# Performance work log

Hardware: AMD Instinct MI355X
Metric: run time of the kernel (lower is better)

Reference implementation:

```python
import jax, jax.numpy as jnp
import numpy as np

B, S, DIM = 8, 1, 2048
H = 16
QLR, KVLR = 1536, 512
DN, DR, DV = 128, 64, 128      # qk_nope, qk_rope, v head dims
START = 8191                    # start_pos; end_pos = START + S = 8192
EPS = 1e-6
SCALE = (DN + DR) ** -0.5


def _rms(x, w):
    # F.rms_norm: x / sqrt(mean(x^2)+eps) * w
    return x * w * jax.lax.rsqrt(jnp.mean(jnp.square(x), axis=-1, keepdims=True) + EPS)


def _rope(x, cos, sin):
    # x: [..., r]; consecutive pairs (x0,x1) treated as complex, multiplied by cos+i*sin
    xr, xi = x[..., 0::2], x[..., 1::2]
    out_r = xr * cos - xi * sin
    out_i = xr * sin + xi * cos
    return jnp.stack([out_r, out_i], axis=-1).reshape(x.shape)


def setup_inputs() -> dict:
    key = jax.random.key(0)
    ks = jax.random.split(key, 12)
    # rotary tables for the single decode position
    inv_freq = 1.0 / (10000.0 ** (np.arange(0, DR, 2, dtype=np.float32) / DR))  # [DR/2]
    pos = np.arange(START, START + S, dtype=np.float32)[:, None]                # [S,1]
    ang = pos * inv_freq[None, :]                                               # [S, DR/2]
    return {
        "x": jax.random.normal(ks[0], (B, S, DIM), jnp.float32),
        "start_pos": START,
        "freqs_cos": jnp.asarray(np.cos(ang)),
        "freqs_sin": jnp.asarray(np.sin(ang)),
        "kv_cache_prefix": jax.random.normal(ks[1], (B, START, KVLR), jnp.float32),
        "pe_cache_prefix": jax.random.normal(ks[2], (B, START, DR), jnp.float32),
        "wq_a_w": jax.random.normal(ks[3], (QLR, DIM), jnp.float32) * 0.02,
        "wq_a_b": jnp.zeros((QLR,), jnp.float32),
        "q_norm_w": jnp.ones((QLR,), jnp.float32),
        "wq_b_w": jax.random.normal(ks[4], (H * (DN + DR), QLR), jnp.float32) * 0.02,
        "wq_b_b": jnp.zeros((H * (DN + DR),), jnp.float32),
        "wkv_a_w": jax.random.normal(ks[5], (KVLR + DR, DIM), jnp.float32) * 0.02,
        "wkv_a_b": jnp.zeros((KVLR + DR,), jnp.float32),
        "kv_norm_w": jnp.ones((KVLR,), jnp.float32),
        "wkv_b_w": jax.random.normal(ks[6], (H * (DN + DV), KVLR), jnp.float32) * 0.02,
        "wo_w": jax.random.normal(ks[7], (DIM, H * DV), jnp.float32) * 0.02,
        "wo_b": jnp.zeros((DIM,), jnp.float32),
    }


def reference(x, start_pos, freqs_cos, freqs_sin, kv_cache_prefix, pe_cache_prefix,
              wq_a_w, wq_a_b, q_norm_w, wq_b_w, wq_b_b,
              wkv_a_w, wkv_a_b, kv_norm_w, wkv_b_w, wo_w, wo_b):
    b, s, _ = x.shape
    # low-rank query projection
    q = _rms(x @ wq_a_w.T + wq_a_b, q_norm_w) @ wq_b_w.T + wq_b_b
    q = q.reshape(b, s, H, DN + DR)
    q_nope, q_pe = q[..., :DN], q[..., DN:]
    cos = freqs_cos[None, :, None, :]  # [1,s,1,DR/2]
    sin = freqs_sin[None, :, None, :]
    q_pe = _rope(q_pe, cos, sin)
    # compressed KV + rope key branch
    kvpe = x @ wkv_a_w.T + wkv_a_b               # [b,s,KVLR+DR]
    kv, k_pe = kvpe[..., :KVLR], kvpe[..., KVLR:]
    k_pe = _rope(k_pe[:, :, None, :], cos, sin)[:, :, 0, :]
    # weight absorption: project q_nope into latent space through wkv_b's K-part
    wkv_b = wkv_b_w.reshape(H, DN + DV, KVLR)
    q_abs = jnp.einsum('bshd,hdc->bshc', q_nope, wkv_b[:, :DN])
    # append current step to caches
    kv_cache = jnp.concatenate([kv_cache_prefix, _rms(kv, kv_norm_w)], axis=1)  # [b,t,KVLR]
    pe_cache = jnp.concatenate([pe_cache_prefix, k_pe], axis=1)                 # [b,t,DR]
    # attention in latent space (seqlen=1 decode -> no causal mask needed)
    scores = (jnp.einsum('bshc,btc->bsht', q_abs, kv_cache)
              + jnp.einsum('bshr,btr->bsht', q_pe, pe_cache)) * SCALE
    attn = jax.nn.softmax(scores.astype(jnp.float32), axis=-1).astype(x.dtype)
    out = jnp.einsum('bsht,btc->bshc', attn, kv_cache)
    out = jnp.einsum('bshc,hdc->bshd', out, wkv_b[:, DN:])  # V-part of wkv_b
    return out.reshape(b, s, H * DV) @ wo_w.T + wo_b
```

## Files before the change

kernel.cpp:

```cpp
#include <hip/hip_runtime.h>
#include <math.h>

namespace {
constexpr int B_   = 8;
constexpr int DIM_ = 2048;
constexpr int H_   = 16;
constexpr int QLR_ = 1536;
constexpr int KVLR_= 512;
constexpr int DN_  = 128;
constexpr int DR_  = 64;
constexpr int DV_  = 128;
constexpr int TPRE_= 8191;
constexpr int CE_  = 576;
constexpr int NCH_ = 32;
constexpr int CT_  = 256;
constexpr int TS_  = 32;
constexpr int PSTR_= 20;
constexpr float EPS_ = 1e-6f;
constexpr float SCALE_ = 0.07216878364870322f;

constexpr size_t WS_QLAT  = 0;
constexpr size_t WS_KVPE  = WS_QLAT  + (size_t)B_*QLR_;
constexpr size_t WS_KVNEW = WS_KVPE  + (size_t)B_*CE_;
constexpr size_t WS_PENEW = WS_KVNEW + (size_t)B_*KVLR_;
constexpr size_t WS_SSQ   = WS_PENEW + (size_t)B_*DR_;
constexpr size_t WS_QNOPE = WS_SSQ   + 16;
constexpr size_t WS_QT    = WS_QNOPE + (size_t)B_*H_*DN_;
constexpr size_t WS_MLOC  = WS_QT    + (size_t)B_*CE_*H_;
constexpr size_t WS_LLOC  = WS_MLOC  + (size_t)B_*H_*NCH_;
constexpr size_t WS_OUT2  = WS_LLOC  + (size_t)B_*H_*NCH_;
constexpr size_t WS_OPART = WS_OUT2  + (size_t)B_*DIM_;
}

__device__ __forceinline__ void gload16(const float* src, float* ldsDst) {
  __builtin_amdgcn_global_load_lds((const __attribute__((address_space(1))) void*)src,
                                   (__attribute__((address_space(3))) void*)ldsDst,
                                   16, 0, 0);
}

__device__ __forceinline__ float rsum16(float v) {
  int x = __float_as_int(v);
  v += __int_as_float(__builtin_amdgcn_update_dpp(0, x, 0xB1, 0xF, 0xF, true));
  x = __float_as_int(v);
  v += __int_as_float(__builtin_amdgcn_update_dpp(0, x, 0x4E, 0xF, 0xF, true));
  x = __float_as_int(v);
  v += __int_as_float(__builtin_amdgcn_update_dpp(0, x, 0x141, 0xF, 0xF, true));
  x = __float_as_int(v);
  v += __int_as_float(__builtin_amdgcn_update_dpp(0, x, 0x140, 0xF, 0xF, true));
  return v;
}

__global__ __launch_bounds__(256) void mla_k1(const float* __restrict__ x,
                                              const float* __restrict__ wqa,
                                              const float* __restrict__ bqa,
                                              const float* __restrict__ wkva,
                                              const float* __restrict__ bkva,
                                              const float* __restrict__ fcos,
                                              const float* __restrict__ fsin,
                                              float* __restrict__ ws) {
  __shared__ float red[4 * B_];
  const int w = threadIdx.x >> 6, l = threadIdx.x & 63;
  const int r0 = (blockIdx.x * 4 + w) * 2;
  const float* W; const float* bias; int rr;
  if (r0 < QLR_) { W = wqa;  bias = bqa;  rr = r0; }
  else           { W = wkva; bias = bkva; rr = r0 - QLR_; }
  const float4* w0p = (const float4*)(W + (size_t)rr * DIM_);
  const float4* w1p = (const float4*)(W + (size_t)(rr + 1) * DIM_);
  const float4* x4  = (const float4*)x;
  float4 wv0[8], wv1[8];
#pragma unroll
  for (int j = 0; j < 8; ++j) { wv0[j] = w0p[l + 64 * j]; wv1[j] = w1p[l + 64 * j]; }
  float acc0[B_], acc1[B_];
#pragma unroll
  for (int b = 0; b < B_; ++b) { acc0[b] = 0.f; acc1[b] = 0.f; }
#pragma unroll
  for (int b = 0; b < B_; ++b) {
#pragma unroll
    for (int j = 0; j < 8; ++j) {
      const float4 xv = x4[b * (DIM_ / 4) + l + 64 * j];
      acc0[b] = fmaf(wv0[j].x, xv.x, fmaf(wv0[j].y, xv.y, fmaf(wv0[j].z, xv.z, fmaf(wv0[j].w, xv.w, acc0[b]))));
      acc1[b] = fmaf(wv1[j].x, xv.x, fmaf(wv1[j].y, xv.y, fmaf(wv1[j].z, xv.z, fmaf(wv1[j].w, xv.w, acc1[b]))));
    }
  }
#pragma unroll
  for (int b = 0; b < B_; ++b)
#pragma unroll
    for (int s = 32; s; s >>= 1) {
      acc0[b] += __shfl_xor(acc0[b], s);
      acc1[b] += __shfl_xor(acc1[b], s);
    }
  const int rblk = blockIdx.x * 8;
  if (l == 0) {
    const float b0 = bias[rr], b1 = bias[rr + 1];
    if (r0 < QLR_) {
      float* out = ws + WS_QLAT;
#pragma unroll
      for (int b = 0; b < B_; ++b) {
        const float v0 = acc0[b] + b0, v1 = acc1[b] + b1;
        out[b * QLR_ + r0]     = v0;
        out[b * QLR_ + r0 + 1] = v1;
        red[w * B_ + b] = v0 * v0 + v1 * v1;
      }
    } else if (rr < KVLR_) {
      float* out = ws + WS_KVPE;
#pragma unroll
      for (int b = 0; b < B_; ++b) {
        const float v0 = acc0[b] + b0, v1 = acc1[b] + b1;
        out[b * CE_ + rr]     = v0;
        out[b * CE_ + rr + 1] = v1;
        red[w * B_ + b] = v0 * v0 + v1 * v1;
      }
    } else {
      const int i = (rr - KVLR_) >> 1;
      const float c = fcos[i], s = fsin[i];
      float* pen = ws + WS_PENEW;
#pragma unroll
      for (int b = 0; b < B_; ++b) {
        const float xr = acc0[b] + b0, xi = acc1[b] + b1;
        pen[b * DR_ + 2 * i]     = xr * c - xi * s;
        pen[b * DR_ + 2 * i + 1] = xr * s + xi * c;
      }
    }
  }
  if (rblk < QLR_ + KVLR_) {
    __syncthreads();
    if (threadIdx.x < B_) {
      const float sacc = red[0 * B_ + threadIdx.x] + red[1 * B_ + threadIdx.x] +
                         red[2 * B_ + threadIdx.x] + red[3 * B_ + threadIdx.x];
      atomicAdd(&ws[WS_SSQ + (rblk >= QLR_ ? B_ : 0) + threadIdx.x], sacc);
    }
  }
}

__global__ __launch_bounds__(256) void mla_k3(const float* __restrict__ qnw,
                                              const float* __restrict__ wqb,
                                              const float* __restrict__ bqb,
                                              const float* __restrict__ fcos,
                                              const float* __restrict__ fsin,
                                              float* __restrict__ ws) {
  const int w = threadIdx.x >> 6, l = threadIdx.x & 63;
  const int r0 = blockIdx.x * 8 + w * 2;
  const float4* w0p = (const float4*)(wqb + (size_t)r0 * QLR_);
  const float4* w1p = (const float4*)(wqb + (size_t)(r0 + 1) * QLR_);
  const float4* g4  = (const float4*)qnw;
  const float4* x4  = (const float4*)(ws + WS_QLAT);
  float4 wg0[6], wg1[6];
#pragma unroll
  for (int j = 0; j < 6; ++j) {
    const int c4 = l + 64 * j;
    const float4 a = w0p[c4], bb = w1p[c4], g = g4[c4];
    wg0[j].x = a.x * g.x; wg0[j].y = a.y * g.y; wg0[j].z = a.z * g.z; wg0[j].w = a.w * g.w;
    wg1[j].x = bb.x * g.x; wg1[j].y = bb.y * g.y; wg1[j].z = bb.z * g.z; wg1[j].w = bb.w * g.w;
  }
  float acc0[B_], acc1[B_];
#pragma unroll
  for (int b = 0; b < B_; ++b) { acc0[b] = 0.f; acc1[b] = 0.f; }
#pragma unroll
  for (int b = 0; b < B_; ++b) {
#pragma unroll
    for (int j = 0; j < 6; ++j) {
      const float4 xv = x4[b * (QLR_ / 4) + l + 64 * j];
      acc0[b] = fmaf(wg0[j].x, xv.x, fmaf(wg0[j].y, xv.y, fmaf(wg0[j].z, xv.z, fmaf(wg0[j].w, xv.w, acc0[b]))));
      acc1[b] = fmaf(wg1[j].x, xv.x, fmaf(wg1[j].y, xv.y, fmaf(wg1[j].z, xv.z, fmaf(wg1[j].w, xv.w, acc1[b]))));
    }
  }
#pragma unroll
  for (int b = 0; b < B_; ++b)
#pragma unroll
    for (int s = 32; s; s >>= 1) {
      acc0[b] += __shfl_xor(acc0[b], s);
      acc1[b] += __shfl_xor(acc1[b], s);
    }
  if (l == 0) {
    const int h = r0 / (DN_ + DR_);
    const int j0 = r0 - h * (DN_ + DR_);
    const float b0 = bqb[r0], b1 = bqb[r0 + 1];
    if (j0 < DN_) {
      float* qn = ws + WS_QNOPE;
#pragma unroll
      for (int b = 0; b < B_; ++b) {
        const float sb = 1.0f / sqrtf(ws[WS_SSQ + b] / (float)QLR_ + EPS_);
        qn[(b * H_ + h) * DN_ + j0]     = acc0[b] * sb + b0;
        qn[(b * H_ + h) * DN_ + j0 + 1] = acc1[b] * sb + b1;
      }
    } else {
      const int i = (j0 - DN_) >> 1;
      const float c = fcos[i], s = fsin[i];
      float* qTT = ws + WS_QT;
#pragma unroll
      for (int b = 0; b < B_; ++b) {
        const float sb = 1.0f / sqrtf(ws[WS_SSQ + b] / (float)QLR_ + EPS_);
        const float xr = acc0[b] * sb + b0, xi = acc1[b] * sb + b1;
        qTT[((size_t)(b * H_ + h)) * CE_ + KVLR_ + 2 * i]     = xr * c - xi * s;
        qTT[((size_t)(b * H_ + h)) * CE_ + KVLR_ + 2 * i + 1] = xr * s + xi * c;
      }
    }
  }
}

__global__ __launch_bounds__(256) void mla_k4(const float* __restrict__ wkvb,
                                              float* __restrict__ ws) {
  __shared__ float red[7 * 32 * B_];
  const int h = blockIdx.y;
  const int strip = blockIdx.x;
  const int tid = threadIdx.x;
  const int c = tid & 31, dg = tid >> 5;
  const int cg = strip * 32 + c;
  const float* qn = ws + WS_QNOPE;
  float acc[B_];
#pragma unroll
  for (int b = 0; b < B_; ++b) acc[b] = 0.f;
  const float* wp = wkvb + (size_t)h * 256 * KVLR_ + cg;
#pragma unroll
  for (int dd = 0; dd < 16; ++dd) {
    const int d = dg * 16 + dd;
    const float wv = wp[(size_t)d * KVLR_];
#pragma unroll
    for (int b = 0; b < B_; ++b) acc[b] = fmaf(qn[(b * H_ + h) * DN_ + d], wv, acc[b]);
  }
  if (dg > 0) {
#pragma unroll
    for (int b = 0; b < B_; ++b) red[(((dg - 1) * 32) + c) * B_ + b] = acc[b];
  }
  __syncthreads();
  if (dg == 0) {
    float* qTT = ws + WS_QT;
#pragma unroll
    for (int b = 0; b < B_; ++b) {
      float v = acc[b];
#pragma unroll
      for (int g = 0; g < 7; ++g) v += red[(g * 32 + c) * B_ + b];
      qTT[((size_t)(b * H_ + h)) * CE_ + cg] = v;
    }
  }
}

__global__ __launch_bounds__(512) void mla_k5(const float* __restrict__ kvpre,
                                              const float* __restrict__ pepre,
                                              const float* __restrict__ kvnw,
                                              float* __restrict__ ws) {
  __shared__ float kv_lds[2][TS_ * CE_];
  __shared__ float p_lds[TS_ * PSTR_];
  __shared__ float m_st[H_], l_st[H_], f_st[H_];

  const int b = blockIdx.y, chunk = blockIdx.x;
  const int t0 = chunk * CT_;
  const int tid = threadIdx.x;
  const int w = tid >> 6, l = tid & 63;
  const int cs = l & 15;
  const int hl = l >> 4;
  const int tg = w >> 1;
  const int hg = (w & 1) * 4 + hl;
  const int c4p = tid >> 2, h4p = tid & 3;

  const float* kvraw = ws + WS_KVPE + b * CE_;
  const float* penew = ws + WS_PENEW + b * DR_;

  auto stageKV = [&](float* buf, int s) {
    const int ts0 = t0 + s * TS_;
#pragma unroll
    for (int k = 0; k < 9; ++k) {
      const int i = w + 8 * k;
      const int f = i * 64 + l;
      const int tl = f / 144;
      const int c4 = f - tl * 144;
      const int tgl = ts0 + tl;
      const float* src;
      if (tgl < TPRE_) {
        src = (c4 < 128) ? (kvpre + ((size_t)b * TPRE_ + tgl) * KVLR_ + 4 * c4)
                         : (pepre + ((size_t)b * TPRE_ + tgl) * DR_ + 4 * (c4 - 128));
      } else {
        src = (c4 < 128) ? (kvraw + 4 * c4) : (penew + 4 * (c4 - 128));
      }
      gload16(src, buf + (size_t)i * 64 * 4);
    }
  };

  stageKV(kv_lds[0], 0);

  float4 q0v[9], q1v[9];
  {
    const float* qb0 = ws + WS_QT + ((size_t)(b * H_) + 2 * hg) * CE_ + cs * 36;
    const float* qb1 = qb0 + CE_;
#pragma unroll
    for (int j = 0; j < 9; ++j) {
      q0v[j] = *(const float4*)(qb0 + 4 * j);
      q1v[j] = *(const float4*)(qb1 + 4 * j);
    }
  }
  if (tid < H_) { m_st[tid] = -3.4e38f; l_st[tid] = 0.f; }

  float o[4][4];
#pragma unroll
  for (int cc = 0; cc < 4; ++cc)
#pragma unroll
    for (int hh = 0; hh < 4; ++hh) o[cc][hh] = 0.f;

  for (int s = 0; s < CT_ / TS_; ++s) {
    __syncthreads();
    if (s + 1 < CT_ / TS_) stageKV(kv_lds[(s + 1) & 1], s + 1);
    float* bufc = kv_lds[s & 1];

    if (chunk == NCH_ - 1 && s == CT_ / TS_ - 1) {
      const float sck = 1.0f / sqrtf(ws[WS_SSQ + B_ + b] / (float)KVLR_ + EPS_);
      float* row = bufc + (TS_ - 1) * CE_;
      row[tid] = row[tid] * kvnw[tid] * sck;
      __syncthreads();
    }

    {
      const float* kb = bufc + (tg * 8) * CE_ + cs * 36;
#pragma unroll
      for (int tt = 0; tt < 8; ++tt) {
        const float* kr = kb + tt * CE_;
        float a0 = 0.f, a1 = 0.f;
#pragma unroll
        for (int j = 0; j < 9; ++j) {
          const float4 k = *(const float4*)(kr + 4 * j);
          const float4 qa = q0v[j], qc = q1v[j];
          a0 = fmaf(k.x, qa.x, fmaf(k.y, qa.y, fmaf(k.z, qa.z, fmaf(k.w, qa.w, a0))));
          a1 = fmaf(k.x, qc.x, fmaf(k.y, qc.y, fmaf(k.z, qc.z, fmaf(k.w, qc.w, a1))));
        }
        a0 = rsum16(a0);
        a1 = rsum16(a1);
        if (cs == 0) {
          float2 v; v.x = a0 * SCALE_; v.y = a1 * SCALE_;
          *(float2*)(p_lds + (tg * 8 + tt) * PSTR_ + 2 * hg) = v;
        }
      }
    }
    __syncthreads();

    {
      const int h2 = tid >> 5, tl2 = tid & 31;
      const float sv = p_lds[tl2 * PSTR_ + h2];
      float msub = sv;
#pragma unroll
      for (int d = 16; d; d >>= 1) msub = fmaxf(msub, __shfl_xor(msub, d, 32));
      const float mold = m_st[h2];
      const float mnew = fmaxf(mold, msub);
      const float e = __expf(sv - mnew);
      float lsum = e;
#pragma unroll
      for (int d = 16; d; d >>= 1) lsum += __shfl_xor(lsum, d, 32);
      p_lds[tl2 * PSTR_ + h2] = e;
      if (tl2 == 0) {
        const float fac = __expf(mold - mnew);
        f_st[h2] = fac;
        l_st[h2] = l_st[h2] * fac + lsum;
        m_st[h2] = mnew;
      }
    }
    __syncthreads();

    {
      const float4 fv = *(const float4*)(f_st + 4 * h4p);
#pragma unroll
      for (int cc = 0; cc < 4; ++cc) {
        o[cc][0] *= fv.x; o[cc][1] *= fv.y; o[cc][2] *= fv.z; o[cc][3] *= fv.w;
      }
#pragma unroll 8
      for (int t = 0; t < TS_; ++t) {
        const float4 kq = *(const float4*)(bufc + t * CE_ + 4 * c4p);
        const float4 pq = *(const float4*)(p_lds + t * PSTR_ + 4 * h4p);
        o[0][0] = fmaf(pq.x, kq.x, o[0][0]); o[0][1] = fmaf(pq.y, kq.x, o[0][1]);
        o[0][2] = fmaf(pq.z, kq.x, o[0][2]); o[0][3] = fmaf(pq.w, kq.x, o[0][3]);
        o[1][0] = fmaf(pq.x, kq.y, o[1][0]); o[1][1] = fmaf(pq.y, kq.y, o[1][1]);
        o[1][2] = fmaf(pq.z, kq.y, o[1][2]); o[1][3] = fmaf(pq.w, kq.y, o[1][3]);
        o[2][0] = fmaf(pq.x, kq.z, o[2][0]); o[2][1] = fmaf(pq.y, kq.z, o[2][1]);
        o[2][2] = fmaf(pq.z, kq.z, o[2][2]); o[2][3] = fmaf(pq.w, kq.z, o[2][3]);
        o[3][0] = fmaf(pq.x, kq.w, o[3][0]); o[3][1] = fmaf(pq.y, kq.w, o[3][1]);
        o[3][2] = fmaf(pq.z, kq.w, o[3][2]); o[3][3] = fmaf(pq.w, kq.w, o[3][3]);
      }
    }
  }

  {
    float* Op = ws + WS_OPART;
#pragma unroll
    for (int hh = 0; hh < 4; ++hh) {
      const int h = 4 * h4p + hh;
      float4 v;
      v.x = o[0][hh]; v.y = o[1][hh]; v.z = o[2][hh]; v.w = o[3][hh];
      *(float4*)(Op + ((size_t)(b * H_ + h) * NCH_ + chunk) * KVLR_ + 4 * c4p) = v;
    }
    if (tid < H_) {
      ws[WS_MLOC + (b * H_ + tid) * NCH_ + chunk] = m_st[tid];
      ws[WS_LLOC + (b * H_ + tid) * NCH_ + chunk] = l_st[tid];
    }
  }
}

__global__ __launch_bounds__(256) void mla_k6(const float* __restrict__ wkvb,
                                              float* __restrict__ ws) {
  const int h = blockIdx.x, b = blockIdx.y;
  __shared__ float wgt[NCH_];
  __shared__ float ao[KVLR_];
  __shared__ float Linv;
  const int tid = threadIdx.x;
  if (tid < NCH_) {
    const float m = ws[WS_MLOC + (b * H_ + h) * NCH_ + tid];
    float M = m;
#pragma unroll
    for (int s = 16; s; s >>= 1) M = fmaxf(M, __shfl_xor(M, s, 32));
    const float wv = __expf(m - M);
    wgt[tid] = wv;
    float lv = ws[WS_LLOC + (b * H_ + h) * NCH_ + tid] * wv;
#pragma unroll
    for (int s = 16; s; s >>= 1) lv += __shfl_xor(lv, s, 32);
    if (tid == 0) Linv = 1.0f / lv;
  }
  __syncthreads();
  const float* Ob = ws + WS_OPART + (size_t)(b * H_ + h) * NCH_ * KVLR_;
  float s0 = 0.f, s1 = 0.f;
#pragma unroll 4
  for (int i = 0; i < NCH_; ++i) {
    const float wv = wgt[i];
    s0 = fmaf(wv, Ob[(size_t)i * KVLR_ + tid], s0);
    s1 = fmaf(wv, Ob[(size_t)i * KVLR_ + tid + 256], s1);
  }
  const float li = Linv;
  ao[tid] = s0 * li;
  ao[tid + 256] = s1 * li;
  __syncthreads();

  const int w6 = tid >> 6, l6 = tid & 63;
  const float4 ax = *(const float4*)(ao + 4 * l6);
  const float4 bx = *(const float4*)(ao + 256 + 4 * l6);
  float* out2 = ws + WS_OUT2 + b * DIM_ + h * DV_;
#pragma unroll 2
  for (int k = 0; k < 32; k += 2) {
    const int v0 = w6 * 32 + k;
    const float4* w20 = (const float4*)(wkvb + ((size_t)h * 256 + DN_ + v0) * KVLR_);
    const float4* w21 = (const float4*)(wkvb + ((size_t)h * 256 + DN_ + v0 + 1) * KVLR_);
    const float4 a0 = w20[l6], c0 = w20[64 + l6];
    const float4 a1 = w21[l6], c1 = w21[64 + l6];
    float t0 = fmaf(a0.x, ax.x, fmaf(a0.y, ax.y, fmaf(a0.z, ax.z, fmaf(a0.w, ax.w,
               fmaf(c0.x, bx.x, fmaf(c0.y, bx.y, fmaf(c0.z, bx.z, c0.w * bx.w)))))));
    float t1 = fmaf(a1.x, ax.x, fmaf(a1.y, ax.y, fmaf(a1.z, ax.z, fmaf(a1.w, ax.w,
               fmaf(c1.x, bx.x, fmaf(c1.y, bx.y, fmaf(c1.z, bx.z, c1.w * bx.w)))))));
#pragma unroll
    for (int d = 32; d; d >>= 1) {
      t0 += __shfl_xor(t0, d);
      t1 += __shfl_xor(t1, d);
    }
    if (l6 == 0) { out2[v0] = t0; out2[v0 + 1] = t1; }
  }
}

__global__ __launch_bounds__(256) void mla_k7(const float* __restrict__ wo,
                                              const float* __restrict__ wob,
                                              const float* __restrict__ ws,
                                              float* __restrict__ out) {
  const int w = threadIdx.x >> 6, l = threadIdx.x & 63;
  const int r0 = (blockIdx.x * 4 + w) * 2;
  const float4* w0p = (const float4*)(wo + (size_t)r0 * DIM_);
  const float4* w1p = (const float4*)(wo + (size_t)(r0 + 1) * DIM_);
  const float4* x4  = (const float4*)(ws + WS_OUT2);
  float4 wv0[8], wv1[8];
#pragma unroll
  for (int j = 0; j < 8; ++j) { wv0[j] = w0p[l + 64 * j]; wv1[j] = w1p[l + 64 * j]; }
  float acc0[B_], acc1[B_];
#pragma unroll
  for (int b = 0; b < B_; ++b) { acc0[b] = 0.f; acc1[b] = 0.f; }
#pragma unroll
  for (int b = 0; b < B_; ++b) {
#pragma unroll
    for (int j = 0; j < 8; ++j) {
      const float4 xv = x4[b * (DIM_ / 4) + l + 64 * j];
      acc0[b] = fmaf(wv0[j].x, xv.x, fmaf(wv0[j].y, xv.y, fmaf(wv0[j].z, xv.z, fmaf(wv0[j].w, xv.w, acc0[b]))));
      acc1[b] = fmaf(wv1[j].x, xv.x, fmaf(wv1[j].y, xv.y, fmaf(wv1[j].z, xv.z, fmaf(wv1[j].w, xv.w, acc1[b]))));
    }
  }
#pragma unroll
  for (int b = 0; b < B_; ++b)
#pragma unroll
    for (int s = 32; s; s >>= 1) {
      acc0[b] += __shfl_xor(acc0[b], s);
      acc1[b] += __shfl_xor(acc1[b], s);
    }
  if (l == 0) {
    const float b0 = wob[r0], b1 = wob[r0 + 1];
#pragma unroll
    for (int b = 0; b < B_; ++b) {
      out[b * DIM_ + r0]     = acc0[b] + b0;
      out[b * DIM_ + r0 + 1] = acc1[b] + b1;
    }
  }
}

extern "C" void kernel_launch(void* const* d_in, const int* in_sizes, int n_in,
                              void* d_out, int out_size, void* d_ws, size_t ws_size,
                              hipStream_t stream) {
  (void)in_sizes; (void)n_in; (void)out_size; (void)ws_size;
  const float* x     = (const float*)d_in[0];
  const float* fcos  = (const float*)d_in[2];
  const float* fsin  = (const float*)d_in[3];
  const float* kvpre = (const float*)d_in[4];
  const float* pepre = (const float*)d_in[5];
  const float* wqa   = (const float*)d_in[6];
  const float* bqa   = (const float*)d_in[7];
  const float* qnw   = (const float*)d_in[8];
  const float* wqb   = (const float*)d_in[9];
  const float* bqb   = (const float*)d_in[10];
  const float* wkva  = (const float*)d_in[11];
  const float* bkva  = (const float*)d_in[12];
  const float* kvnw  = (const float*)d_in[13];
  const float* wkvb  = (const float*)d_in[14];
  const float* wo    = (const float*)d_in[15];
  const float* wob   = (const float*)d_in[16];
  float* ws  = (float*)d_ws;
  float* out = (float*)d_out;

  hipMemsetAsync((char*)d_ws + WS_SSQ * sizeof(float), 0, 16 * sizeof(float), stream);
  mla_k1<<<dim3((QLR_ + CE_) / 8), dim3(256), 0, stream>>>(x, wqa, bqa, wkva, bkva, fcos, fsin, ws);
  mla_k3<<<dim3(H_ * (DN_ + DR_) / 8), dim3(256), 0, stream>>>(qnw, wqb, bqb, fcos, fsin, ws);
  mla_k4<<<dim3(16, H_), dim3(256), 0, stream>>>(wkvb, ws);
  mla_k5<<<dim3(NCH_, B_), dim3(512), 0, stream>>>(kvpre, pepre, kvnw, ws);
  mla_k6<<<dim3(H_, B_), dim3(256), 0, stream>>>(wkvb, ws);
  mla_k7<<<dim3(DIM_ / 8), dim3(256), 0, stream>>>(wo, wob, ws, out);
}
```

Before: 351.2 us.

## Double attention chunk count and recompute RMS norms locally instead of atomics

The attention split-K kernel now uses 64 chunks of 128 tokens with 16-token stages, doubling the number of blocks over the KV cache to raise parallelism and shrink LDS per stage. The RMS sum-of-squares atomics and the memset are removed; instead each consumer block recomputes the q and kv norm scales from the workspace. Some barriers are replaced with a lighter lgkm-wait barrier. The trade-offs are redundant norm reductions in every block and more partials to merge in the combine kernel.

```diff
diff --git a/kernel.cpp b/kernel.cpp
--- a/kernel.cpp
+++ b/kernel.cpp
@@ -12,19 +12,18 @@
 constexpr int DV_  = 128;
 constexpr int TPRE_= 8191;
 constexpr int CE_  = 576;
-constexpr int NCH_ = 32;
-constexpr int CT_  = 256;
-constexpr int TS_  = 32;
+constexpr int NCH_ = 64;
+constexpr int CT_  = 128;
+constexpr int TS_  = 16;
+constexpr int NS_  = CT_ / TS_;
 constexpr int PSTR_= 20;
 constexpr float EPS_ = 1e-6f;
 constexpr float SCALE_ = 0.07216878364870322f;
 
 constexpr size_t WS_QLAT  = 0;
 constexpr size_t WS_KVPE  = WS_QLAT  + (size_t)B_*QLR_;
-constexpr size_t WS_KVNEW = WS_KVPE  + (size_t)B_*CE_;
-constexpr size_t WS_PENEW = WS_KVNEW + (size_t)B_*KVLR_;
-constexpr size_t WS_SSQ   = WS_PENEW + (size_t)B_*DR_;
-constexpr size_t WS_QNOPE = WS_SSQ   + 16;
+constexpr size_t WS_PENEW = WS_KVPE  + (size_t)B_*CE_;
+constexpr size_t WS_QNOPE = WS_PENEW + (size_t)B_*DR_;
 constexpr size_t WS_QT    = WS_QNOPE + (size_t)B_*H_*DN_;
 constexpr size_t WS_MLOC  = WS_QT    + (size_t)B_*CE_*H_;
 constexpr size_t WS_LLOC  = WS_MLOC  + (size_t)B_*H_*NCH_;
@@ -50,6 +49,12 @@
   return v;
 }
 
+__device__ __forceinline__ void barrier_lgkm() {
+  asm volatile("s_waitcnt lgkmcnt(0)" ::: "memory");
+  __builtin_amdgcn_s_barrier();
+  __builtin_amdgcn_sched_barrier(0);
+}
+
 __global__ __launch_bounds__(256) void mla_k1(const float* __restrict__ x,
                                               const float* __restrict__ wqa,
                                               const float* __restrict__ bqa,
@@ -58,7 +63,6 @@
                                               const float* __restrict__ fcos,
                                               const float* __restrict__ fsin,
                                               float* __restrict__ ws) {
-  __shared__ float red[4 * B_];
   const int w = threadIdx.x >> 6, l = threadIdx.x & 63;
   const int r0 = (blockIdx.x * 4 + w) * 2;
   const float* W; const float* bias; int rr;
@@ -89,26 +93,21 @@
       acc0[b] += __shfl_xor(acc0[b], s);
       acc1[b] += __shfl_xor(acc1[b], s);
     }
-  const int rblk = blockIdx.x * 8;
   if (l == 0) {
     const float b0 = bias[rr], b1 = bias[rr + 1];
     if (r0 < QLR_) {
       float* out = ws + WS_QLAT;
 #pragma unroll
       for (int b = 0; b < B_; ++b) {
-        const float v0 = acc0[b] + b0, v1 = acc1[b] + b1;
-        out[b * QLR_ + r0]     = v0;
-        out[b * QLR_ + r0 + 1] = v1;
-        red[w * B_ + b] = v0 * v0 + v1 * v1;
+        out[b * QLR_ + r0]     = acc0[b] + b0;
+        out[b * QLR_ + r0 + 1] = acc1[b] + b1;
       }
     } else if (rr < KVLR_) {
       float* out = ws + WS_KVPE;
 #pragma unroll
       for (int b = 0; b < B_; ++b) {
-        const float v0 = acc0[b] + b0, v1 = acc1[b] + b1;
-        out[b * CE_ + rr]     = v0;
-        out[b * CE_ + rr + 1] = v1;
-        red[w * B_ + b] = v0 * v0 + v1 * v1;
+        out[b * CE_ + rr]     = acc0[b] + b0;
+        out[b * CE_ + rr + 1] = acc1[b] + b1;
       }
     } else {
       const int i = (rr - KVLR_) >> 1;
@@ -120,14 +119,6 @@
         pen[b * DR_ + 2 * i]     = xr * c - xi * s;
         pen[b * DR_ + 2 * i + 1] = xr * s + xi * c;
       }
-    }
-  }
-  if (rblk < QLR_ + KVLR_) {
-    __syncthreads();
-    if (threadIdx.x < B_) {
-      const float sacc = red[0 * B_ + threadIdx.x] + red[1 * B_ + threadIdx.x] +
-                         red[2 * B_ + threadIdx.x] + red[3 * B_ + threadIdx.x];
-      atomicAdd(&ws[WS_SSQ + (rblk >= QLR_ ? B_ : 0) + threadIdx.x], sacc);
     }
   }
 }
@@ -138,7 +129,23 @@
                                               const float* __restrict__ fcos,
                                               const float* __restrict__ fsin,
                                               float* __restrict__ ws) {
-  const int w = threadIdx.x >> 6, l = threadIdx.x & 63;
+  __shared__ float qs_s[B_];
+  const int tid = threadIdx.x;
+  {
+    const int bq = tid >> 5, l32 = tid & 31;
+    const float4* ql4 = (const float4*)(ws + WS_QLAT + (size_t)bq * QLR_);
+    float ss = 0.f;
+#pragma unroll
+    for (int j = 0; j < 12; ++j) {
+      const float4 v = ql4[l32 + 32 * j];
+      ss = fmaf(v.x, v.x, fmaf(v.y, v.y, fmaf(v.z, v.z, fmaf(v.w, v.w, ss))));
+    }
+#pragma unroll
+    for (int d = 16; d; d >>= 1) ss += __shfl_xor(ss, d, 32);
+    if (l32 == 0) qs_s[bq] = 1.0f / sqrtf(ss / (float)QLR_ + EPS_);
+    __syncthreads();
+  }
+  const int w = tid >> 6, l = tid & 63;
   const int r0 = blockIdx.x * 8 + w * 2;
   const float4* w0p = (const float4*)(wqb + (size_t)r0 * QLR_);
   const float4* w1p = (const float4*)(wqb + (size_t)(r0 + 1) * QLR_);
@@ -179,7 +186,7 @@
       float* qn = ws + WS_QNOPE;
 #pragma unroll
       for (int b = 0; b < B_; ++b) {
-        const float sb = 1.0f / sqrtf(ws[WS_SSQ + b] / (float)QLR_ + EPS_);
+        const float sb = qs_s[b];
         qn[(b * H_ + h) * DN_ + j0]     = acc0[b] * sb + b0;
         qn[(b * H_ + h) * DN_ + j0 + 1] = acc1[b] * sb + b1;
       }
@@ -189,7 +196,7 @@
       float* qTT = ws + WS_QT;
 #pragma unroll
       for (int b = 0; b < B_; ++b) {
-        const float sb = 1.0f / sqrtf(ws[WS_SSQ + b] / (float)QLR_ + EPS_);
+        const float sb = qs_s[b];
         const float xr = acc0[b] * sb + b0, xi = acc1[b] * sb + b1;
         qTT[((size_t)(b * H_ + h)) * CE_ + KVLR_ + 2 * i]     = xr * c - xi * s;
         qTT[((size_t)(b * H_ + h)) * CE_ + KVLR_ + 2 * i + 1] = xr * s + xi * c;
@@ -242,6 +249,8 @@
   __shared__ float kv_lds[2][TS_ * CE_];
   __shared__ float p_lds[TS_ * PSTR_];
   __shared__ float m_st[H_], l_st[H_], f_st[H_];
+  __shared__ float redw[8];
+  __shared__ float kvs_s;
 
   const int b = blockIdx.y, chunk = blockIdx.x;
   const int t0 = chunk * CT_;
@@ -259,24 +268,40 @@
   auto stageKV = [&](float* buf, int s) {
     const int ts0 = t0 + s * TS_;
 #pragma unroll
-    for (int k = 0; k < 9; ++k) {
-      const int i = w + 8 * k;
-      const int f = i * 64 + l;
-      const int tl = f / 144;
-      const int c4 = f - tl * 144;
-      const int tgl = ts0 + tl;
-      const float* src;
-      if (tgl < TPRE_) {
-        src = (c4 < 128) ? (kvpre + ((size_t)b * TPRE_ + tgl) * KVLR_ + 4 * c4)
-                         : (pepre + ((size_t)b * TPRE_ + tgl) * DR_ + 4 * (c4 - 128));
-      } else {
-        src = (c4 < 128) ? (kvraw + 4 * c4) : (penew + 4 * (c4 - 128));
-      }
-      gload16(src, buf + (size_t)i * 64 * 4);
+    for (int k = 0; k < 5; ++k) {
+      const int i = tid + 512 * k;
+      if (i < (TS_ * CE_) / 4) {
+        const int tl = i / 144;
+        const int c4 = i - tl * 144;
+        const int tgl = ts0 + tl;
+        const float* src;
+        if (tgl < TPRE_) {
+          src = (c4 < 128) ? (kvpre + ((size_t)b * TPRE_ + tgl) * KVLR_ + 4 * c4)
+                           : (pepre + ((size_t)b * TPRE_ + tgl) * DR_ + 4 * (c4 - 128));
+        } else {
+          src = (c4 < 128) ? (kvraw + 4 * c4) : (penew + 4 * (c4 - 128));
+        }
+        gload16(src, buf + (size_t)i * 4);
+      }
     }
   };
 
   stageKV(kv_lds[0], 0);
+
+  {
+    const float v = ws[WS_KVPE + b * CE_ + tid];
+    float ss = v * v;
+#pragma unroll
+    for (int d = 32; d; d >>= 1) ss += __shfl_xor(ss, d);
+    if (l == 0) redw[w] = ss;
+    __syncthreads();
+    if (tid == 0) {
+      float s = 0.f;
+#pragma unroll
+      for (int g = 0; g < 8; ++g) s += redw[g];
+      kvs_s = 1.0f / sqrtf(s / (float)KVLR_ + EPS_);
+    }
+  }
 
   float4 q0v[9], q1v[9];
   {
@@ -296,22 +321,21 @@
 #pragma unroll
     for (int hh = 0; hh < 4; ++hh) o[cc][hh] = 0.f;
 
-  for (int s = 0; s < CT_ / TS_; ++s) {
+  for (int s = 0; s < NS_; ++s) {
     __syncthreads();
-    if (s + 1 < CT_ / TS_) stageKV(kv_lds[(s + 1) & 1], s + 1);
+    if (s + 1 < NS_) stageKV(kv_lds[(s + 1) & 1], s + 1);
     float* bufc = kv_lds[s & 1];
 
-    if (chunk == NCH_ - 1 && s == CT_ / TS_ - 1) {
-      const float sck = 1.0f / sqrtf(ws[WS_SSQ + B_ + b] / (float)KVLR_ + EPS_);
+    if (chunk == NCH_ - 1 && s == NS_ - 1) {
       float* row = bufc + (TS_ - 1) * CE_;
-      row[tid] = row[tid] * kvnw[tid] * sck;
+      row[tid] = row[tid] * kvnw[tid] * kvs_s;
       __syncthreads();
     }
 
     {
-      const float* kb = bufc + (tg * 8) * CE_ + cs * 36;
-#pragma unroll
-      for (int tt = 0; tt < 8; ++tt) {
+      const float* kb = bufc + (tg * 4) * CE_ + cs * 36;
+#pragma unroll
+      for (int tt = 0; tt < 4; ++tt) {
         const float* kr = kb + tt * CE_;
         float a0 = 0.f, a1 = 0.f;
 #pragma unroll
@@ -325,24 +349,24 @@
         a1 = rsum16(a1);
         if (cs == 0) {
           float2 v; v.x = a0 * SCALE_; v.y = a1 * SCALE_;
-          *(float2*)(p_lds + (tg * 8 + tt) * PSTR_ + 2 * hg) = v;
+          *(float2*)(p_lds + (tg * 4 + tt) * PSTR_ + 2 * hg) = v;
         }
       }
     }
-    __syncthreads();
-
-    {
-      const int h2 = tid >> 5, tl2 = tid & 31;
+    barrier_lgkm();
+
+    if (tid < 256) {
+      const int h2 = tid >> 4, tl2 = tid & 15;
       const float sv = p_lds[tl2 * PSTR_ + h2];
       float msub = sv;
 #pragma unroll
-      for (int d = 16; d; d >>= 1) msub = fmaxf(msub, __shfl_xor(msub, d, 32));
+      for (int d = 8; d; d >>= 1) msub = fmaxf(msub, __shfl_xor(msub, d, 16));
       const float mold = m_st[h2];
       const float mnew = fmaxf(mold, msub);
       const float e = __expf(sv - mnew);
       float lsum = e;
 #pragma unroll
-      for (int d = 16; d; d >>= 1) lsum += __shfl_xor(lsum, d, 32);
+      for (int d = 8; d; d >>= 1) lsum += __shfl_xor(lsum, d, 16);
       p_lds[tl2 * PSTR_ + h2] = e;
       if (tl2 == 0) {
         const float fac = __expf(mold - mnew);
@@ -351,7 +375,7 @@
         m_st[h2] = mnew;
       }
     }
-    __syncthreads();
+    barrier_lgkm();
 
     {
       const float4 fv = *(const float4*)(f_st + 4 * h4p);
@@ -402,12 +426,12 @@
     const float m = ws[WS_MLOC + (b * H_ + h) * NCH_ + tid];
     float M = m;
 #pragma unroll
-    for (int s = 16; s; s >>= 1) M = fmaxf(M, __shfl_xor(M, s, 32));
+    for (int s = 32; s; s >>= 1) M = fmaxf(M, __shfl_xor(M, s));
     const float wv = __expf(m - M);
     wgt[tid] = wv;
     float lv = ws[WS_LLOC + (b * H_ + h) * NCH_ + tid] * wv;
 #pragma unroll
-    for (int s = 16; s; s >>= 1) lv += __shfl_xor(lv, s, 32);
+    for (int s = 32; s; s >>= 1) lv += __shfl_xor(lv, s);
     if (tid == 0) Linv = 1.0f / lv;
   }
   __syncthreads();
@@ -512,7 +536,6 @@
   float* ws  = (float*)d_ws;
   float* out = (float*)d_out;
 
-  hipMemsetAsync((char*)d_ws + WS_SSQ * sizeof(float), 0, 16 * sizeof(float), stream);
   mla_k1<<<dim3((QLR_ + CE_) / 8), dim3(256), 0, stream>>>(x, wqa, bqa, wkva, bkva, fcos, fsin, ws);
   mla_k3<<<dim3(H_ * (DN_ + DR_) / 8), dim3(256), 0, stream>>>(qnw, wqb, bqb, fcos, fsin, ws);
   mla_k4<<<dim3(16, H_), dim3(256), 0, stream>>>(wkvb, ws);
```

New measurement: 354.4 us. Within noise of the previous version (+0.9%).
